# Optimization experiments

Hardware: AMD Instinct MI355X
Metric: run time of the kernel (lower is better)

## Reference

```python
import jax, jax.numpy as jnp
import numpy as np

MA_K = 2 * 125 + 1  # 251, moving-average kernel
MV_K = 4 * 125 + 1  # 501, moving-variance kernel
EPS = 1e-5


def _avg_pool1d(x, K):
    """PyTorch F.avg_pool1d(stride=1, padding=(K-1)//2, count_include_pad=True)
    computed in O(L) via prefix sums. x: (B, C, L) -> (B, C, L)."""
    pad = (K - 1) // 2
    xp = jnp.pad(x, ((0, 0), (0, 0), (pad, pad)))  # zero pad, length L+K-1
    c = jnp.pad(jnp.cumsum(xp, axis=-1), ((0, 0), (0, 0), (1, 0)))  # length L+K
    return (c[..., K:] - c[..., :-K]) / K  # divide by K always (count_include_pad)


def setup_inputs() -> dict:
    key = jax.random.key(0)
    x = jax.random.normal(key, (8192, 1, 3750), dtype=jnp.float32)
    return {"x": x}


def reference(x):
    # global z-norm per (batch, channel); torch.std is unbiased (ddof=1)
    x = (x - jnp.mean(x, axis=2, keepdims=True)) / (
        jnp.std(x, axis=2, keepdims=True, ddof=1) + EPS)
    # remove moving average (kernel 251)
    x = x - _avg_pool1d(x, MA_K)
    # rescale by moving std (kernel 501)
    x = x / (jnp.sqrt(_avg_pool1d(x * x, MV_K)) + EPS)
    return x
```

## Files before the change

kernel.cpp:

```cpp
#include <hip/hip_runtime.h>
#include <math.h>

namespace {

constexpr int L      = 3750;
constexpr int NPAIR  = L / 2;
constexpr int BLK    = 256;
constexpr int CH     = 15;
constexpr int NCHUNK = L / CH;
constexpr float EPS  = 1e-5f;

__device__ __forceinline__ float frcp(float x)  { return __builtin_amdgcn_rcpf(x); }
__device__ __forceinline__ float fsqrt(float x) { return __builtin_amdgcn_sqrtf(x); }

__global__ __launch_bounds__(BLK, 8)
void preproc_kernel(const float* __restrict__ in, float* __restrict__ out) {
    __shared__ __align__(16) float sp[L + 1];
    __shared__ float sred[8];

    const int tid  = threadIdx.x;
    const int lane = tid & 63;
    const int wave = tid >> 6;
    const size_t rowoff = (size_t)blockIdx.x * (size_t)L;
    const float* rin  = in  + rowoff;
    float*       rout = out + rowoff;

    {
        const float2* rin2 = reinterpret_cast<const float2*>(rin);
        float2* sp2 = reinterpret_cast<float2*>(sp);
        for (int i = tid; i < NPAIR; i += BLK) sp2[i] = rin2[i];
    }
    __syncthreads();

    float y[CH];
    float cy = 0.f, cy2 = 0.f;
    const int base = tid * CH;
    if (tid < NCHUNK) {
        #pragma unroll
        for (int j = 0; j < CH; ++j) {
            const float v = sp[base + j];
            y[j] = v;
            cy  += v;
            cy2 += v * v;
        }
    }
    float iy = cy, iy2 = cy2;
    #pragma unroll
    for (int d = 1; d < 64; d <<= 1) {
        const float u  = __shfl_up(iy,  (unsigned)d, 64);
        const float u2 = __shfl_up(iy2, (unsigned)d, 64);
        if (lane >= d) { iy += u; iy2 += u2; }
    }
    if (lane == 63) { sred[wave] = iy; sred[4 + wave] = iy2; }
    __syncthreads();
    float woff = 0.f;
    for (int w = 0; w < wave; ++w) woff += sred[w];
    const float totY  = sred[0] + sred[1] + sred[2] + sred[3];
    const float totY2 = sred[4] + sred[5] + sred[6] + sred[7];
    const float mean  = totY * (1.f / (float)L);
    const float var   = (totY2 - totY * mean) * (1.f / (float)(L - 1));
    const float zinv  = frcp(fsqrt(var) + EPS);

    {
        float run = woff + iy - cy;
        if (tid < NCHUNK) {
            #pragma unroll
            for (int j = 0; j < CH; ++j) { sp[base + j] = run; run += y[j]; }
            if (tid == NCHUNK - 1) sp[L] = run;
        }
    }
    __syncthreads();

    float ct = 0.f;
    {
        const float zinv251 = zinv * (1.f / 251.f);
        if (tid < NCHUNK) {
            #pragma unroll
            for (int j = 0; j < CH; ++j) {
                const int i  = base + j;
                const int lo = (i > 125) ? (i - 125) : 0;
                const int hi = (i + 126 < L) ? (i + 126) : L;
                const float winY = sp[hi] - sp[lo] - (float)(hi - lo) * mean;
                const float z    = (y[j] - mean) * zinv;
                const float t    = z - winY * zinv251;
                y[j] = t;
                ct  += t * t;
            }
        }
    }
    float it = ct;
    #pragma unroll
    for (int d = 1; d < 64; d <<= 1) {
        const float u = __shfl_up(it, (unsigned)d, 64);
        if (lane >= d) it += u;
    }
    if (lane == 63) sred[wave] = it;
    __syncthreads();
    float woff2 = 0.f;
    for (int w = 0; w < wave; ++w) woff2 += sred[w];

    {
        float run = woff2 + it - ct;
        if (tid < NCHUNK) {
            #pragma unroll
            for (int j = 0; j < CH; ++j) { sp[base + j] = run; run += y[j] * y[j]; }
            if (tid == NCHUNK - 1) sp[L] = run;
        }
    }
    __syncthreads();

    {
        const float inv501 = 1.f / 501.f;
        if (tid < NCHUNK) {
            #pragma unroll
            for (int j = 0; j < CH; ++j) {
                const int i  = base + j;
                const int lo = (i > 250) ? (i - 250) : 0;
                const int hi = (i + 251 < L) ? (i + 251) : L;
                float mv = (sp[hi] - sp[lo]) * inv501;
                mv = fmaxf(mv, 0.f);
                y[j] = y[j] * frcp(fsqrt(mv) + EPS);
            }
        }
    }
    __syncthreads();

    if (tid < NCHUNK) {
        #pragma unroll
        for (int j = 0; j < CH; ++j) sp[base + j] = y[j];
    }
    __syncthreads();
    {
        const float2* sp2 = reinterpret_cast<const float2*>(sp);
        float2* rout2 = reinterpret_cast<float2*>(rout);
        for (int i = tid; i < NPAIR; i += BLK) rout2[i] = sp2[i];
    }
}

}

extern "C" void kernel_launch(void* const* d_in, const int* in_sizes, int n_in,
                              void* d_out, int out_size, void* d_ws, size_t ws_size,
                              hipStream_t stream) {
    const float* x = (const float*)d_in[0];
    float* out = (float*)d_out;
    const int rows = in_sizes[0] / L;
    preproc_kernel<<<rows, BLK, 0, stream>>>(x, out);
}
```

Baseline: 52.75 us.

## Load rows straight into registers and vectorize interior prefix-window reads

Each thread now reads and writes its 16-element chunk directly from and to global memory with float2 accesses, instead of staging the row through shared memory. This removes the LDS copy-in and copy-out passes and two barriers. Interior threads read the prefix-sum windows with aligned float4 loads, and the mean correction is folded away because interior windows always have full length; boundary threads keep the clamped scalar path. The trade-offs are per-thread strided global accesses that coalesce less well, a lower occupancy hint, and more register pressure.

```diff
diff --git a/kernel.cpp b/kernel.cpp
--- a/kernel.cpp
+++ b/kernel.cpp
@@ -3,19 +3,19 @@
 
 namespace {
 
-constexpr int L      = 3750;
-constexpr int NPAIR  = L / 2;
-constexpr int BLK    = 256;
-constexpr int CH     = 15;
-constexpr int NCHUNK = L / CH;
-constexpr float EPS  = 1e-5f;
+constexpr int   L      = 3750;
+constexpr int   BLK    = 256;
+constexpr int   CH     = 16;
+constexpr int   NCHUNK = (L + CH - 1) / CH;
+constexpr int   PADE   = NCHUNK * CH;
+constexpr float EPS    = 1e-5f;
 
 __device__ __forceinline__ float frcp(float x)  { return __builtin_amdgcn_rcpf(x); }
 __device__ __forceinline__ float fsqrt(float x) { return __builtin_amdgcn_sqrtf(x); }
 
-__global__ __launch_bounds__(BLK, 8)
+__global__ __launch_bounds__(BLK, 6)
 void preproc_kernel(const float* __restrict__ in, float* __restrict__ out) {
-    __shared__ __align__(16) float sp[L + 1];
+    __shared__ __align__(16) float sp[PADE];
     __shared__ float sred[8];
 
     const int tid  = threadIdx.x;
@@ -25,25 +25,32 @@
     const float* rin  = in  + rowoff;
     float*       rout = out + rowoff;
 
-    {
-        const float2* rin2 = reinterpret_cast<const float2*>(rin);
-        float2* sp2 = reinterpret_cast<float2*>(sp);
-        for (int i = tid; i < NPAIR; i += BLK) sp2[i] = rin2[i];
-    }
-    __syncthreads();
+    const bool active = (tid < NCHUNK);
+    const bool full   = (tid < NCHUNK - 1);
+    const int  base   = tid * CH;
 
     float y[CH];
+    #pragma unroll
+    for (int j = 0; j < CH; ++j) y[j] = 0.f;
+    if (full) {
+        const float2* g = reinterpret_cast<const float2*>(rin + base);
+        #pragma unroll
+        for (int h = 0; h < CH / 2; ++h) {
+            const float2 v = g[h];
+            y[2*h] = v.x; y[2*h+1] = v.y;
+        }
+    } else if (active) {
+        const float2* g = reinterpret_cast<const float2*>(rin + base);
+        #pragma unroll
+        for (int h = 0; h < 3; ++h) {
+            const float2 v = g[h];
+            y[2*h] = v.x; y[2*h+1] = v.y;
+        }
+    }
+
     float cy = 0.f, cy2 = 0.f;
-    const int base = tid * CH;
-    if (tid < NCHUNK) {
-        #pragma unroll
-        for (int j = 0; j < CH; ++j) {
-            const float v = sp[base + j];
-            y[j] = v;
-            cy  += v;
-            cy2 += v * v;
-        }
-    }
+    #pragma unroll
+    for (int j = 0; j < CH; ++j) { cy += y[j]; cy2 = fmaf(y[j], y[j], cy2); }
     float iy = cy, iy2 = cy2;
     #pragma unroll
     for (int d = 1; d < 64; d <<= 1) {
@@ -54,40 +61,78 @@
     if (lane == 63) { sred[wave] = iy; sred[4 + wave] = iy2; }
     __syncthreads();
     float woff = 0.f;
-    for (int w = 0; w < wave; ++w) woff += sred[w];
+    #pragma unroll
+    for (int w = 0; w < 4; ++w) if (w < wave) woff += sred[w];
     const float totY  = sred[0] + sred[1] + sred[2] + sred[3];
     const float totY2 = sred[4] + sred[5] + sred[6] + sred[7];
     const float mean  = totY * (1.f / (float)L);
     const float var   = (totY2 - totY * mean) * (1.f / (float)(L - 1));
     const float zinv  = frcp(fsqrt(var) + EPS);
 
-    {
+    if (active) {
         float run = woff + iy - cy;
-        if (tid < NCHUNK) {
-            #pragma unroll
-            for (int j = 0; j < CH; ++j) { sp[base + j] = run; run += y[j]; }
-            if (tid == NCHUNK - 1) sp[L] = run;
-        }
-    }
-    __syncthreads();
+        float4* q = reinterpret_cast<float4*>(sp + base);
+        #pragma unroll
+        for (int h = 0; h < CH / 4; ++h) {
+            float4 w;
+            w.x = run; run += y[4*h+0];
+            w.y = run; run += y[4*h+1];
+            w.z = run; run += y[4*h+2];
+            w.w = run; run += y[4*h+3];
+            q[h] = w;
+        }
+    }
+    __syncthreads();
+
+    const float inv251  = 1.f / 251.f;
+    const float zinv251 = zinv * inv251;
+    if (active) {
+        if (tid >= 8 && tid <= 225) {
+            float d[CH];
+            {
+                const float4* q = reinterpret_cast<const float4*>(sp + base - 128);
+                float a[20];
+                #pragma unroll
+                for (int h = 0; h < 5; ++h) {
+                    const float4 v = q[h];
+                    a[4*h]=v.x; a[4*h+1]=v.y; a[4*h+2]=v.z; a[4*h+3]=v.w;
+                }
+                #pragma unroll
+                for (int j = 0; j < CH; ++j) d[j] = -a[3 + j];
+            }
+            {
+                const float4* q = reinterpret_cast<const float4*>(sp + base + 124);
+                float a[20];
+                #pragma unroll
+                for (int h = 0; h < 5; ++h) {
+                    const float4 v = q[h];
+                    a[4*h]=v.x; a[4*h+1]=v.y; a[4*h+2]=v.z; a[4*h+3]=v.w;
+                }
+                #pragma unroll
+                for (int j = 0; j < CH; ++j) d[j] += a[2 + j];
+            }
+            #pragma unroll
+            for (int j = 0; j < CH; ++j)
+                y[j] = zinv * fmaf(d[j], -inv251, y[j]);
+        } else {
+            #pragma unroll
+            for (int j = 0; j < CH; ++j) {
+                const int i = base + j;
+                if (i < L) {
+                    const int lo = (i > 125) ? i - 125 : 0;
+                    const int hi = (i + 126 < L) ? i + 126 : L;
+                    const float winY = sp[hi] - sp[lo] - (float)(hi - lo) * mean;
+                    y[j] = (y[j] - mean) * zinv - winY * zinv251;
+                } else {
+                    y[j] = 0.f;
+                }
+            }
+        }
+    }
 
     float ct = 0.f;
-    {
-        const float zinv251 = zinv * (1.f / 251.f);
-        if (tid < NCHUNK) {
-            #pragma unroll
-            for (int j = 0; j < CH; ++j) {
-                const int i  = base + j;
-                const int lo = (i > 125) ? (i - 125) : 0;
-                const int hi = (i + 126 < L) ? (i + 126) : L;
-                const float winY = sp[hi] - sp[lo] - (float)(hi - lo) * mean;
-                const float z    = (y[j] - mean) * zinv;
-                const float t    = z - winY * zinv251;
-                y[j] = t;
-                ct  += t * t;
-            }
-        }
-    }
+    #pragma unroll
+    for (int j = 0; j < CH; ++j) ct = fmaf(y[j], y[j], ct);
     float it = ct;
     #pragma unroll
     for (int d = 1; d < 64; d <<= 1) {
@@ -97,43 +142,82 @@
     if (lane == 63) sred[wave] = it;
     __syncthreads();
     float woff2 = 0.f;
-    for (int w = 0; w < wave; ++w) woff2 += sred[w];
-
-    {
+    #pragma unroll
+    for (int w = 0; w < 4; ++w) if (w < wave) woff2 += sred[w];
+    if (active) {
         float run = woff2 + it - ct;
-        if (tid < NCHUNK) {
-            #pragma unroll
-            for (int j = 0; j < CH; ++j) { sp[base + j] = run; run += y[j] * y[j]; }
-            if (tid == NCHUNK - 1) sp[L] = run;
-        }
-    }
-    __syncthreads();
-
-    {
-        const float inv501 = 1.f / 501.f;
-        if (tid < NCHUNK) {
+        float4* q = reinterpret_cast<float4*>(sp + base);
+        #pragma unroll
+        for (int h = 0; h < CH / 4; ++h) {
+            float4 w;
+            w.x = run; run = fmaf(y[4*h+0], y[4*h+0], run);
+            w.y = run; run = fmaf(y[4*h+1], y[4*h+1], run);
+            w.z = run; run = fmaf(y[4*h+2], y[4*h+2], run);
+            w.w = run; run = fmaf(y[4*h+3], y[4*h+3], run);
+            q[h] = w;
+        }
+    }
+    __syncthreads();
+
+    const float inv501 = 1.f / 501.f;
+    if (active) {
+        if (tid >= 16 && tid <= 217) {
+            float d[CH];
+            {
+                const float4* q = reinterpret_cast<const float4*>(sp + base - 252);
+                float a[20];
+                #pragma unroll
+                for (int h = 0; h < 5; ++h) {
+                    const float4 v = q[h];
+                    a[4*h]=v.x; a[4*h+1]=v.y; a[4*h+2]=v.z; a[4*h+3]=v.w;
+                }
+                #pragma unroll
+                for (int j = 0; j < CH; ++j) d[j] = -a[2 + j];
+            }
+            {
+                const float4* q = reinterpret_cast<const float4*>(sp + base + 248);
+                float a[20];
+                #pragma unroll
+                for (int h = 0; h < 5; ++h) {
+                    const float4 v = q[h];
+                    a[4*h]=v.x; a[4*h+1]=v.y; a[4*h+2]=v.z; a[4*h+3]=v.w;
+                }
+                #pragma unroll
+                for (int j = 0; j < CH; ++j) d[j] += a[3 + j];
+            }
             #pragma unroll
             for (int j = 0; j < CH; ++j) {
-                const int i  = base + j;
-                const int lo = (i > 250) ? (i - 250) : 0;
-                const int hi = (i + 251 < L) ? (i + 251) : L;
-                float mv = (sp[hi] - sp[lo]) * inv501;
+                float mv = d[j] * inv501;
                 mv = fmaxf(mv, 0.f);
                 y[j] = y[j] * frcp(fsqrt(mv) + EPS);
             }
-        }
-    }
-    __syncthreads();
-
-    if (tid < NCHUNK) {
-        #pragma unroll
-        for (int j = 0; j < CH; ++j) sp[base + j] = y[j];
-    }
-    __syncthreads();
-    {
-        const float2* sp2 = reinterpret_cast<const float2*>(sp);
-        float2* rout2 = reinterpret_cast<float2*>(rout);
-        for (int i = tid; i < NPAIR; i += BLK) rout2[i] = sp2[i];
+        } else {
+            #pragma unroll
+            for (int j = 0; j < CH; ++j) {
+                const int i = base + j;
+                if (i < L) {
+                    const int lo = (i > 250) ? i - 250 : 0;
+                    const int hi = (i + 251 < L) ? i + 251 : L;
+                    float mv = (sp[hi] - sp[lo]) * inv501;
+                    mv = fmaxf(mv, 0.f);
+                    y[j] = y[j] * frcp(fsqrt(mv) + EPS);
+                }
+            }
+        }
+        float2* gout = reinterpret_cast<float2*>(rout + base);
+        if (full) {
+            #pragma unroll
+            for (int h = 0; h < CH / 2; ++h) {
+                float2 v; v.x = y[2*h]; v.y = y[2*h+1];
+                gout[h] = v;
+            }
+        } else {
+            #pragma unroll
+            for (int h = 0; h < 3; ++h) {
+                float2 v; v.x = y[2*h]; v.y = y[2*h+1];
+                gout[h] = v;
+            }
+        }
     }
 }
 
```

After: 110.1 us. 2.09x slower.

## Process each row with a single wavefront and vectorized LDS window reads

Applied to the files above, without the earlier changes.

Changes the block from 256 threads to one 64-lane wavefront per row, with each lane owning 60 elements. Cross-wave scans through shared memory and their barriers are replaced by wave shuffles only. Window sums for interior chunks now use float4 LDS loads of the neighbouring prefix values, with a scalar fallback kept for the edges. The z-normalisation is folded algebraically into the epsilon of the final scale, which removes a multiply per element. In exchange, each thread holds many more registers and there are fewer threads per row to hide latency, which can lower occupancy.

```diff
diff --git a/kernel.cpp b/kernel.cpp
--- a/kernel.cpp
+++ b/kernel.cpp
@@ -3,137 +3,209 @@
 
 namespace {
 
-constexpr int L      = 3750;
-constexpr int NPAIR  = L / 2;
-constexpr int BLK    = 256;
-constexpr int CH     = 15;
-constexpr int NCHUNK = L / CH;
-constexpr float EPS  = 1e-5f;
+constexpr int   L     = 3750;
+constexpr int   NPAIR = L / 2;
+constexpr int   CH    = 60;
+constexpr int   PADL  = 64 * CH;
+constexpr int   TAIL  = NPAIR - 29 * 64;
+constexpr int   ZPAIR = PADL / 2 - NPAIR;
+constexpr float EPS   = 1e-5f;
 
 __device__ __forceinline__ float frcp(float x)  { return __builtin_amdgcn_rcpf(x); }
 __device__ __forceinline__ float fsqrt(float x) { return __builtin_amdgcn_sqrtf(x); }
 
-__global__ __launch_bounds__(BLK, 8)
+__global__ __launch_bounds__(64)
 void preproc_kernel(const float* __restrict__ in, float* __restrict__ out) {
-    __shared__ __align__(16) float sp[L + 1];
-    __shared__ float sred[8];
-
-    const int tid  = threadIdx.x;
-    const int lane = tid & 63;
-    const int wave = tid >> 6;
+    __shared__ __align__(16) float sp[PADL];
+
+    const int lane = threadIdx.x;
     const size_t rowoff = (size_t)blockIdx.x * (size_t)L;
     const float* rin  = in  + rowoff;
     float*       rout = out + rowoff;
 
     {
-        const float2* rin2 = reinterpret_cast<const float2*>(rin);
+        const float2* g = reinterpret_cast<const float2*>(rin);
+        float2 v[30];
+        #pragma unroll
+        for (int k = 0; k < 29; ++k) v[k] = g[64 * k + lane];
+        if (lane < TAIL) v[29] = g[64 * 29 + lane];
         float2* sp2 = reinterpret_cast<float2*>(sp);
-        for (int i = tid; i < NPAIR; i += BLK) sp2[i] = rin2[i];
+        #pragma unroll
+        for (int k = 0; k < 29; ++k) sp2[64 * k + lane] = v[k];
+        if (lane < TAIL) sp2[64 * 29 + lane] = v[29];
+        if (lane < ZPAIR) {
+            float2 z; z.x = 0.f; z.y = 0.f;
+            sp2[NPAIR + lane] = z;
+        }
     }
     __syncthreads();
 
     float y[CH];
+    {
+        const float4* q4 = reinterpret_cast<const float4*>(sp);
+        #pragma unroll
+        for (int h = 0; h < 15; ++h) {
+            const float4 v = q4[15 * lane + h];
+            y[4*h+0] = v.x; y[4*h+1] = v.y; y[4*h+2] = v.z; y[4*h+3] = v.w;
+        }
+    }
+
     float cy = 0.f, cy2 = 0.f;
-    const int base = tid * CH;
-    if (tid < NCHUNK) {
-        #pragma unroll
-        for (int j = 0; j < CH; ++j) {
-            const float v = sp[base + j];
-            y[j] = v;
-            cy  += v;
-            cy2 += v * v;
-        }
-    }
-    float iy = cy, iy2 = cy2;
+    #pragma unroll
+    for (int j = 0; j < CH; ++j) { cy += y[j]; cy2 = fmaf(y[j], y[j], cy2); }
+    float iy = cy;
     #pragma unroll
     for (int d = 1; d < 64; d <<= 1) {
-        const float u  = __shfl_up(iy,  (unsigned)d, 64);
-        const float u2 = __shfl_up(iy2, (unsigned)d, 64);
-        if (lane >= d) { iy += u; iy2 += u2; }
-    }
-    if (lane == 63) { sred[wave] = iy; sred[4 + wave] = iy2; }
-    __syncthreads();
-    float woff = 0.f;
-    for (int w = 0; w < wave; ++w) woff += sred[w];
-    const float totY  = sred[0] + sred[1] + sred[2] + sred[3];
-    const float totY2 = sred[4] + sred[5] + sred[6] + sred[7];
-    const float mean  = totY * (1.f / (float)L);
-    const float var   = (totY2 - totY * mean) * (1.f / (float)(L - 1));
-    const float zinv  = frcp(fsqrt(var) + EPS);
-
-    {
-        float run = woff + iy - cy;
-        if (tid < NCHUNK) {
-            #pragma unroll
-            for (int j = 0; j < CH; ++j) { sp[base + j] = run; run += y[j]; }
-            if (tid == NCHUNK - 1) sp[L] = run;
-        }
-    }
-    __syncthreads();
-
-    float ct = 0.f;
-    {
-        const float zinv251 = zinv * (1.f / 251.f);
-        if (tid < NCHUNK) {
-            #pragma unroll
-            for (int j = 0; j < CH; ++j) {
-                const int i  = base + j;
-                const int lo = (i > 125) ? (i - 125) : 0;
-                const int hi = (i + 126 < L) ? (i + 126) : L;
-                const float winY = sp[hi] - sp[lo] - (float)(hi - lo) * mean;
-                const float z    = (y[j] - mean) * zinv;
-                const float t    = z - winY * zinv251;
-                y[j] = t;
-                ct  += t * t;
-            }
-        }
-    }
-    float it = ct;
+        const float u = __shfl_up(iy, (unsigned)d, 64);
+        if (lane >= d) iy += u;
+    }
+    float t2 = cy2;
+    #pragma unroll
+    for (int d = 1; d < 64; d <<= 1) t2 += __shfl_xor(t2, d, 64);
+    const float totY = __shfl(iy, 63, 64);
+    const float mean = totY * (1.f / (float)L);
+    const float var  = (t2 - totY * mean) * (1.f / (float)(L - 1));
+    const float s    = fsqrt(var) + EPS;
+    const float epsS = EPS * s;
+
+    {
+        float run = iy - cy;
+        float4* q4 = reinterpret_cast<float4*>(sp);
+        #pragma unroll
+        for (int h = 0; h < 15; ++h) {
+            float4 w;
+            w.x = run; run += y[4*h+0];
+            w.y = run; run += y[4*h+1];
+            w.z = run; run += y[4*h+2];
+            w.w = run; run += y[4*h+3];
+            q4[15 * lane + h] = w;
+        }
+    }
+    __syncthreads();
+
+    const float inv251 = 1.f / 251.f;
+    #pragma unroll
+    for (int m = 0; m < 3; ++m) {
+        const int i0 = 60 * lane + 20 * m;
+        if (i0 >= 125 && i0 <= 3605) {
+            const float4* q4 = reinterpret_cast<const float4*>(sp);
+            const int qlo = 15 * lane + 5 * m - 32;
+            const int qhi = 15 * lane + 5 * m + 31;
+            float a[24], b[24];
+            #pragma unroll
+            for (int h = 0; h < 6; ++h) {
+                const float4 v = q4[qlo + h];
+                a[4*h]=v.x; a[4*h+1]=v.y; a[4*h+2]=v.z; a[4*h+3]=v.w;
+            }
+            #pragma unroll
+            for (int h = 0; h < 6; ++h) {
+                const float4 v = q4[qhi + h];
+                b[4*h]=v.x; b[4*h+1]=v.y; b[4*h+2]=v.z; b[4*h+3]=v.w;
+            }
+            #pragma unroll
+            for (int j = 0; j < 20; ++j) {
+                const float sumY = b[2 + j] - a[3 + j];
+                y[20*m + j] = fmaf(sumY, -inv251, y[20*m + j]);
+            }
+        } else {
+            #pragma unroll
+            for (int j = 0; j < 20; ++j) {
+                const int i  = i0 + j;
+                const int lo = (i > 125) ? i - 125 : 0;
+                const int hi = (i + 126 < L) ? i + 126 : L;
+                const float sumY = sp[hi] - sp[lo];
+                const float cnt  = (float)(hi - lo);
+                y[20*m + j] = y[20*m + j] - mean - (sumY - cnt * mean) * inv251;
+            }
+        }
+    }
+
+    float cu = 0.f;
+    #pragma unroll
+    for (int j = 0; j < CH; ++j) cu = fmaf(y[j], y[j], cu);
+    float iu = cu;
     #pragma unroll
     for (int d = 1; d < 64; d <<= 1) {
-        const float u = __shfl_up(it, (unsigned)d, 64);
-        if (lane >= d) it += u;
-    }
-    if (lane == 63) sred[wave] = it;
-    __syncthreads();
-    float woff2 = 0.f;
-    for (int w = 0; w < wave; ++w) woff2 += sred[w];
-
-    {
-        float run = woff2 + it - ct;
-        if (tid < NCHUNK) {
-            #pragma unroll
-            for (int j = 0; j < CH; ++j) { sp[base + j] = run; run += y[j] * y[j]; }
-            if (tid == NCHUNK - 1) sp[L] = run;
-        }
-    }
-    __syncthreads();
-
-    {
-        const float inv501 = 1.f / 501.f;
-        if (tid < NCHUNK) {
-            #pragma unroll
-            for (int j = 0; j < CH; ++j) {
-                const int i  = base + j;
-                const int lo = (i > 250) ? (i - 250) : 0;
-                const int hi = (i + 251 < L) ? (i + 251) : L;
-                float mv = (sp[hi] - sp[lo]) * inv501;
-                mv = fmaxf(mv, 0.f);
-                y[j] = y[j] * frcp(fsqrt(mv) + EPS);
-            }
-        }
-    }
-    __syncthreads();
-
-    if (tid < NCHUNK) {
-        #pragma unroll
-        for (int j = 0; j < CH; ++j) sp[base + j] = y[j];
-    }
-    __syncthreads();
+        const float t = __shfl_up(iu, (unsigned)d, 64);
+        if (lane >= d) iu += t;
+    }
+    __syncthreads();
+
+    {
+        float run = iu - cu;
+        float4* q4 = reinterpret_cast<float4*>(sp);
+        #pragma unroll
+        for (int h = 0; h < 15; ++h) {
+            float4 w;
+            w.x = run; run = fmaf(y[4*h+0], y[4*h+0], run);
+            w.y = run; run = fmaf(y[4*h+1], y[4*h+1], run);
+            w.z = run; run = fmaf(y[4*h+2], y[4*h+2], run);
+            w.w = run; run = fmaf(y[4*h+3], y[4*h+3], run);
+            q4[15 * lane + h] = w;
+        }
+    }
+    __syncthreads();
+
+    const float inv501 = 1.f / 501.f;
+    #pragma unroll
+    for (int m = 0; m < 3; ++m) {
+        const int i0 = 60 * lane + 20 * m;
+        if (i0 >= 250 && i0 <= 3480) {
+            const float4* q4 = reinterpret_cast<const float4*>(sp);
+            const int qlo = 15 * lane + 5 * m - 63;
+            const int qhi = 15 * lane + 5 * m + 62;
+            float a[24], b[24];
+            #pragma unroll
+            for (int h = 0; h < 6; ++h) {
+                const float4 v = q4[qlo + h];
+                a[4*h]=v.x; a[4*h+1]=v.y; a[4*h+2]=v.z; a[4*h+3]=v.w;
+            }
+            #pragma unroll
+            for (int h = 0; h < 6; ++h) {
+                const float4 v = q4[qhi + h];
+                b[4*h]=v.x; b[4*h+1]=v.y; b[4*h+2]=v.z; b[4*h+3]=v.w;
+            }
+            #pragma unroll
+            for (int j = 0; j < 20; ++j) {
+                float W = (b[3 + j] - a[2 + j]) * inv501;
+                W = fmaxf(W, 0.f);
+                y[20*m + j] = y[20*m + j] * frcp(fsqrt(W) + epsS);
+            }
+        } else {
+            #pragma unroll
+            for (int j = 0; j < 20; ++j) {
+                const int i  = i0 + j;
+                const int lo = (i > 250) ? i - 250 : 0;
+                const int hi = (i + 251 < L) ? i + 251 : L;
+                float W = (sp[hi] - sp[lo]) * inv501;
+                W = fmaxf(W, 0.f);
+                y[20*m + j] = y[20*m + j] * frcp(fsqrt(W) + epsS);
+            }
+        }
+    }
+    __syncthreads();
+
+    {
+        float4* q4 = reinterpret_cast<float4*>(sp);
+        #pragma unroll
+        for (int h = 0; h < 15; ++h) {
+            float4 v;
+            v.x = y[4*h+0]; v.y = y[4*h+1]; v.z = y[4*h+2]; v.w = y[4*h+3];
+            q4[15 * lane + h] = v;
+        }
+    }
+    __syncthreads();
+
     {
         const float2* sp2 = reinterpret_cast<const float2*>(sp);
-        float2* rout2 = reinterpret_cast<float2*>(rout);
-        for (int i = tid; i < NPAIR; i += BLK) rout2[i] = sp2[i];
+        float2* g = reinterpret_cast<float2*>(rout);
+        float2 v[30];
+        #pragma unroll
+        for (int k = 0; k < 29; ++k) v[k] = sp2[64 * k + lane];
+        if (lane < TAIL) v[29] = sp2[64 * 29 + lane];
+        #pragma unroll
+        for (int k = 0; k < 29; ++k) g[64 * k + lane] = v[k];
+        if (lane < TAIL) g[64 * 29 + lane] = v[29];
     }
 }
 
@@ -145,5 +217,5 @@
     const float* x = (const float*)d_in[0];
     float* out = (float*)d_out;
     const int rows = in_sizes[0] / L;
-    preproc_kernel<<<rows, BLK, 0, stream>>>(x, out);
+    preproc_kernel<<<rows, 64, 0, stream>>>(x, out);
 }
```

After: 66.82 us. 1.27x slower.
